# Optimization experiments

Measured on AMD Instinct MI355X. Metric: run time of the kernel, lower is better.

Reference implementation:

```python
import jax, jax.numpy as jnp
import numpy as np

TEMPERATURE = 8.0  # sqrt(d_head=64), from init_kwargs
NEG_INF = -1e9


def setup_inputs() -> dict:
    key = jax.random.key(0)
    k1, k2, k3, k4 = jax.random.split(key, 4)
    B, H, N, D = 2, 16, 2048, 64
    q = jax.random.normal(k1, (B, H, N, D), dtype=jnp.float32)
    k = jax.random.normal(k2, (B, H, N, D), dtype=jnp.float32)
    v = jax.random.normal(k3, (B, H, N, D), dtype=jnp.float32)
    mask = jax.random.randint(k4, (B, 1, N), 0, 2, dtype=jnp.int32)
    return {"q": q, "k": k, "v": v, "mask": mask}


def reference(q, k, v, mask):
    # scores: [B,H,N,N]
    attn = jnp.einsum("bhqd,bhkd->bhqk", q / TEMPERATURE, k)
    # symmetric padding mask: masked if row OR col token is masked
    m = mask.astype(attn.dtype)            # [B,1,N]
    row = m[:, :, :, None]                 # [B,1,N,1]
    col = m[:, :, None, :]                 # [B,1,1,N]
    sym = 1.0 - (1.0 - row) * (1.0 - col)  # [B,1,N,N], broadcasts over H
    attn = jnp.where(sym == 1.0, NEG_INF, attn)
    attn = jax.nn.softmax(attn, axis=-1)
    output = jnp.einsum("bhqk,bhkd->bhqd", attn, v)
    return output, attn
```

## Files before the change

kernel.cpp:

```cpp
#include <hip/hip_runtime.h>

typedef _Float16 half8 __attribute__((ext_vector_type(8)));
typedef _Float16 half4v __attribute__((ext_vector_type(4)));
typedef _Float16 half2v __attribute__((ext_vector_type(2)));
typedef float f32x4 __attribute__((ext_vector_type(4)));
typedef float f32x16 __attribute__((ext_vector_type(16)));
typedef unsigned int u32;
typedef u32 u32x2 __attribute__((ext_vector_type(2)));
typedef u32 u32x4 __attribute__((ext_vector_type(4)));
typedef int i32x4 __attribute__((ext_vector_type(4)));

#if __has_builtin(__builtin_amdgcn_exp2f)
#define EXP2F(x) __builtin_amdgcn_exp2f(x)
#else
#define EXP2F(x) exp2f(x)
#endif

#define QSCALE (1.44269504088896340736f * 0.125f)
#define NEGBIG (-16384.0f)


__device__ __forceinline__ void gload_lds16(const void* g, void* l) {
    __builtin_amdgcn_global_load_lds(
        (const __attribute__((address_space(1))) u32*)g,
        (__attribute__((address_space(3))) u32*)l, 16, 0, 0);
}

__device__ __forceinline__ void stage_tile16k(const _Float16* g, _Float16* l,
                                              int wid, int lane) {
#pragma unroll
    for (int i = 0; i < 4; ++i) {
        const int base = (wid * 4 + i) * 1024;
        gload_lds16((const char*)g + base + lane * 16, (char*)l + base);
    }
}

__device__ __forceinline__ u32 pkh(float a, float b) {
    half2v h; h[0] = (_Float16)a; h[1] = (_Float16)b;
    return __builtin_bit_cast(u32, h);
}

__device__ __forceinline__ void swap32(u32 &a, u32 &b) {
    asm volatile("v_permlane32_swap_b32 %0, %1" : "+v"(a), "+v"(b));
}


__global__ __launch_bounds__(256, 2)
void prep_kv(const float* __restrict__ kg_, const float* __restrict__ vg_,
             _Float16* __restrict__ kws_, _Float16* __restrict__ vws_)
{
    __shared__ float tile[128 * 68];
    const int tid = threadIdx.x;
    const int bh  = blockIdx.x & 31;
    const int kc  = blockIdx.x >> 5;
    const float* kg = kg_ + ((size_t)bh * 2048 + kc * 128) * 64;
    const float* vg = vg_ + ((size_t)bh * 2048 + kc * 128) * 64;
    _Float16* kt = kws_ + ((size_t)bh * 16 + kc) * 8192;
    _Float16* vt = vws_ + ((size_t)bh * 16 + kc) * 8192;

#pragma unroll
    for (int i = 0; i < 8; ++i) {
        int f = tid + 256 * i;
        int r = f >> 4, c4 = f & 15;
        f32x4 x = *reinterpret_cast<const f32x4*>(kg + r * 64 + c4 * 4);
        *reinterpret_cast<f32x4*>(&tile[r * 68 + c4 * 4]) = x;
    }
    __syncthreads();
#pragma unroll
    for (int i = 0; i < 4; ++i) {
        int s16 = tid + 256 * i;
        int R5 = s16 >> 5;
        int r  = R5 * 4 + ((s16 >> 3) & 3);
        int c  = ((s16 & 7) << 4) ^ ((R5 & 7) << 4);
        int d0 = c >> 1;
        f32x4 x0 = *reinterpret_cast<const f32x4*>(&tile[r * 68 + d0]);
        f32x4 x1 = *reinterpret_cast<const f32x4*>(&tile[r * 68 + d0 + 4]);
        half8 h;
#pragma unroll
        for (int j = 0; j < 4; ++j) { h[j] = (_Float16)x0[j]; h[4 + j] = (_Float16)x1[j]; }
        __builtin_nontemporal_store(h, reinterpret_cast<half8*>(kt + s16 * 8));
    }
    __syncthreads();
#pragma unroll
    for (int i = 0; i < 8; ++i) {
        int f = tid + 256 * i;
        int r = f >> 4, c4 = f & 15;
        f32x4 x = *reinterpret_cast<const f32x4*>(vg + r * 64 + c4 * 4);
        *reinterpret_cast<f32x4*>(&tile[r * 68 + c4 * 4]) = x;
    }
    __syncthreads();
#pragma unroll
    for (int i = 0; i < 4; ++i) {
        int s16 = tid + 256 * i;
        int R5 = s16 >> 5;
        int d  = R5 * 2 + ((s16 >> 4) & 1);
        int c  = ((s16 & 15) << 4) ^ ((R5 & 15) << 4);
        int k0 = c >> 1;
        half8 h;
#pragma unroll
        for (int j = 0; j < 8; ++j) h[j] = (_Float16)tile[(k0 + j) * 68 + d];
        __builtin_nontemporal_store(h, reinterpret_cast<half8*>(vt + s16 * 8));
    }
}

__global__ __launch_bounds__(256, 2)
void attn_sums(const float* __restrict__ qg_, const _Float16* __restrict__ kws_,
               const int* __restrict__ mg_, float* __restrict__ rsums_)
{
    __shared__ _Float16 Kb[2][8192];
    __shared__ float biasF[2048];
    const int tid = threadIdx.x, wid = tid >> 6, lane = tid & 63;
    const int l31 = lane & 31, hi = lane >> 5;
    const int bh = blockIdx.x & 31, qt = blockIdx.x >> 5;
    const int* mg = mg_ + (bh >> 4) * 2048;
    const _Float16* ktiles = kws_ + (size_t)bh * 16 * 8192;

    const float* qrow = qg_ + ((size_t)bh * 2048 + qt * 128 + wid * 32 + l31) * 64;
    half8 qf[4];
#pragma unroll
    for (int ks = 0; ks < 4; ++ks) {
        f32x4 x0 = *reinterpret_cast<const f32x4*>(qrow + ks * 16 + hi * 8);
        f32x4 x1 = *reinterpret_cast<const f32x4*>(qrow + ks * 16 + hi * 8 + 4);
#pragma unroll
        for (int j = 0; j < 4; ++j) {
            qf[ks][j]     = (_Float16)(x0[j] * QSCALE);
            qf[ks][4 + j] = (_Float16)(x1[j] * QSCALE);
        }
    }
#pragma unroll
    for (int i = 0; i < 2; ++i) {
        int j = (tid + 256 * i) * 4;
        i32x4 m = *reinterpret_cast<const i32x4*>(mg + j);
        f32x4 bv;
        bv[0] = m[0] ? NEGBIG : 0.f; bv[1] = m[1] ? NEGBIG : 0.f;
        bv[2] = m[2] ? NEGBIG : 0.f; bv[3] = m[3] ? NEGBIG : 0.f;
        *reinterpret_cast<f32x4*>(&biasF[j]) = bv;
    }
    stage_tile16k(ktiles, Kb[0], wid, lane);
    __syncthreads();

    const int rbK = (l31 >> 2) * 512 + (l31 & 3) * 128;
    const int swK = (l31 >> 2) << 4;

    float lsum = 0.f;
    _Float16 *cur = Kb[0], *nxt = Kb[1];
    for (int kc = 0; kc < 16; ++kc) {
        if (kc < 15) stage_tile16k(ktiles + (size_t)(kc + 1) * 8192, nxt, wid, lane);
        asm volatile("" ::: "memory");
        const char* curb = (const char*)cur;
#pragma unroll
        for (int kb = 0; kb < 4; ++kb) {
            f32x16 acc;
#pragma unroll
            for (int g = 0; g < 4; ++g) {
                f32x4 bv = *reinterpret_cast<const f32x4*>(
                    &biasF[kc * 128 + kb * 32 + g * 8 + hi * 4]);
                acc[4*g+0] = bv[0]; acc[4*g+1] = bv[1];
                acc[4*g+2] = bv[2]; acc[4*g+3] = bv[3];
            }
#pragma unroll
            for (int ks = 0; ks < 4; ++ks) {
                half8 kf = *reinterpret_cast<const half8*>(
                    curb + kb * 4096 + rbK + ((ks * 32 + hi * 16) ^ swK));
                acc = __builtin_amdgcn_mfma_f32_32x32x16_f16(kf, qf[ks], acc, 0, 0, 0);
            }
#pragma unroll
            for (int r = 0; r < 16; ++r) lsum += EXP2F(acc[r]);
        }
        __syncthreads();
        _Float16* t = cur; cur = nxt; nxt = t;
    }
    lsum += __shfl_xor(lsum, 32, 64);
    if (hi == 0)
        rsums_[(size_t)bh * 2048 + qt * 128 + wid * 32 + l31] = lsum;
}

__global__ __launch_bounds__(256, 2)
void attn_main(const float* __restrict__ qg_, const _Float16* __restrict__ kws_,
               const _Float16* __restrict__ vws_, const int* __restrict__ mg_,
               const float* __restrict__ rsums_,
               float* __restrict__ outg_, float* __restrict__ attng_)
{
    __shared__ _Float16 Kb[2][8192];
    __shared__ _Float16 Vb[2][8192];
    __shared__ _Float16 biasH[2048];
    __shared__ _Float16 Pb[4][32][40];
    const int tid = threadIdx.x, wid = tid >> 6, lane = tid & 63;
    const int l31 = lane & 31, hi = lane >> 5;
    const int bh = blockIdx.x & 31, qt = blockIdx.x >> 5;
    const int* mg = mg_ + (bh >> 4) * 2048;
    const _Float16* ktiles = kws_ + (size_t)bh * 16 * 8192;
    const _Float16* vtiles = vws_ + (size_t)bh * 16 * 8192;
    const int qrow_l = qt * 128 + wid * 32 + l31;

    const float* qrow = qg_ + ((size_t)bh * 2048 + qrow_l) * 64;
    half8 qf[4];
#pragma unroll
    for (int ks = 0; ks < 4; ++ks) {
        f32x4 x0 = *reinterpret_cast<const f32x4*>(qrow + ks * 16 + hi * 8);
        f32x4 x1 = *reinterpret_cast<const f32x4*>(qrow + ks * 16 + hi * 8 + 4);
#pragma unroll
        for (int j = 0; j < 4; ++j) {
            qf[ks][j]     = (_Float16)(x0[j] * QSCALE);
            qf[ks][4 + j] = (_Float16)(x1[j] * QSCALE);
        }
    }
#pragma unroll
    for (int i = 0; i < 2; ++i) {
        int j = (tid + 256 * i) * 4;
        i32x4 m = *reinterpret_cast<const i32x4*>(mg + j);
        half4v bv;
        bv[0] = m[0] ? (_Float16)NEGBIG : (_Float16)0.f;
        bv[1] = m[1] ? (_Float16)NEGBIG : (_Float16)0.f;
        bv[2] = m[2] ? (_Float16)NEGBIG : (_Float16)0.f;
        bv[3] = m[3] ? (_Float16)NEGBIG : (_Float16)0.f;
        *reinterpret_cast<half4v*>(&biasH[j]) = bv;
    }

    const float rs = rsums_[(size_t)bh * 2048 + qrow_l];
    const int   rm = mg[qrow_l];
    const bool uni = (rm != 0) || !(rs > 0.f);
    const float rscale = uni ? 0.f : 1.f / rs;
    const float radd   = uni ? (1.0f / 2048.0f) : 0.f;

    stage_tile16k(ktiles, Kb[0], wid, lane);
    stage_tile16k(vtiles, Vb[0], wid, lane);
    __syncthreads();

    f32x16 Oacc0, Oacc1;
#pragma unroll
    for (int r = 0; r < 16; ++r) { Oacc0[r] = 0.f; Oacc1[r] = 0.f; }

    float* attnw = attng_ + ((size_t)bh * 2048 + qt * 128 + wid * 32) * 2048;
    _Float16 *curK = Kb[0], *nxtK = Kb[1], *curV = Vb[0], *nxtV = Vb[1];

    const int rbK = (l31 >> 2) * 512 + (l31 & 3) * 128;
    const int swK = (l31 >> 2) << 4;
    const int rbV = (l31 >> 1) * 512 + (l31 & 1) * 256;
    const int swV = (l31 >> 1) << 4;

    for (int kc = 0; kc < 16; ++kc) {
        if (kc < 15) {
            stage_tile16k(ktiles + (size_t)(kc + 1) * 8192, nxtK, wid, lane);
            stage_tile16k(vtiles + (size_t)(kc + 1) * 8192, nxtV, wid, lane);
        }
        asm volatile("" ::: "memory");
        const char* curKb = (const char*)curK;
        const char* curVb = (const char*)curV;
#pragma unroll
        for (int kb = 0; kb < 4; ++kb) {
            f32x16 acc;
#pragma unroll
            for (int g = 0; g < 4; ++g) {
                half4v bv = *reinterpret_cast<const half4v*>(
                    &biasH[kc * 128 + kb * 32 + g * 8 + hi * 4]);
                acc[4*g+0] = (float)bv[0]; acc[4*g+1] = (float)bv[1];
                acc[4*g+2] = (float)bv[2]; acc[4*g+3] = (float)bv[3];
            }
#pragma unroll
            for (int ks = 0; ks < 4; ++ks) {
                half8 kf = *reinterpret_cast<const half8*>(
                    curKb + kb * 4096 + rbK + ((ks * 32 + hi * 16) ^ swK));
                acc = __builtin_amdgcn_mfma_f32_32x32x16_f16(kf, qf[ks], acc, 0, 0, 0);
            }
            float p[16];
#pragma unroll
            for (int r = 0; r < 16; ++r) p[r] = EXP2F(acc[r]) * rscale + radd;

            u32 wA[4], wB[4];
#pragma unroll
            for (int t = 0; t < 4; ++t) {
                wA[t] = pkh(p[4*t],     p[4*t + 1]);
                wB[t] = pkh(p[4*t + 2], p[4*t + 3]);
            }
#pragma unroll
            for (int t = 0; t < 4; ++t) {
                u32x2 ww; ww[0] = wA[t]; ww[1] = wB[t];
                *reinterpret_cast<u32x2*>(&Pb[wid][l31][t * 8 + 4 * hi]) = ww;
            }
            asm volatile("s_waitcnt lgkmcnt(0)" ::: "memory");
            __builtin_amdgcn_sched_barrier(0);

#pragma unroll
            for (int i8 = 0; i8 < 4; ++i8) {
                int rl = i8 * 8 + (lane >> 3);
                half4v ph = *reinterpret_cast<half4v*>(&Pb[wid][rl][(lane & 7) * 4]);
                f32x4 pf;
                pf[0] = (float)ph[0]; pf[1] = (float)ph[1];
                pf[2] = (float)ph[2]; pf[3] = (float)ph[3];
                __builtin_nontemporal_store(pf, reinterpret_cast<f32x4*>(
                    attnw + (size_t)rl * 2048 + kc * 128 + kb * 32 + (lane & 7) * 4));
            }

#pragma unroll
            for (int s = 0; s < 2; ++s) {
                u32 cA = wA[2*s], dA = wB[2*s], cB = wA[2*s + 1], dB = wB[2*s + 1];
                swap32(cA, cB);
                swap32(dA, dB);
                u32x4 wv; wv[0] = cA; wv[1] = dA; wv[2] = cB; wv[3] = dB;
                half8 af = __builtin_bit_cast(half8, wv);
#pragma unroll
                for (int nd = 0; nd < 2; ++nd) {
                    half8 bf = *reinterpret_cast<const half8*>(
                        curVb + nd * 8192 + rbV +
                        ((kb * 64 + s * 32 + hi * 16) ^ swV));
                    if (nd == 0) Oacc0 = __builtin_amdgcn_mfma_f32_32x32x16_f16(af, bf, Oacc0, 0, 0, 0);
                    else         Oacc1 = __builtin_amdgcn_mfma_f32_32x32x16_f16(af, bf, Oacc1, 0, 0, 0);
                }
            }
        }
        if (kc < 15) {
            asm volatile("s_waitcnt vmcnt(16) lgkmcnt(0)" ::: "memory");
            __builtin_amdgcn_s_barrier();
            _Float16* t;
            t = curK; curK = nxtK; nxtK = t;
            t = curV; curV = nxtV; nxtV = t;
        }
    }

    float* outg = outg_ + ((size_t)bh * 2048 + qt * 128) * 64;
#pragma unroll
    for (int r = 0; r < 16; ++r) {
        int q_l = wid * 32 + (r & 3) + 8 * (r >> 2) + 4 * hi;
        __builtin_nontemporal_store(Oacc0[r], outg + (size_t)q_l * 64 + l31);
        __builtin_nontemporal_store(Oacc1[r], outg + (size_t)q_l * 64 + 32 + l31);
    }
}

__global__ __launch_bounds__(256, 2)
void attn_fused(const float* __restrict__ qg_, const float* __restrict__ kg_,
                const float* __restrict__ vg_, const int* __restrict__ mg_,
                float* __restrict__ outg_, float* __restrict__ attng_)
{
    constexpr int N = 2048, D = 64, TM = 128, BK = 128, NCH = 16;
    constexpr int QS = 72, KS = 72, VTS = 136, PS = 72;
    constexpr float INVN = 1.0f / 2048.0f;

    __shared__ _Float16 Qs[TM * QS];
    __shared__ _Float16 Ksh[BK * KS];
    __shared__ _Float16 Vts[D * VTS];
    __shared__ _Float16 Ps[TM * PS];
    __shared__ unsigned char cm[N];

    const int tid  = threadIdx.x;
    const int wid  = tid >> 6;
    const int lane = tid & 63;
    const int quad = lane >> 4;
    const int l15  = lane & 15;

    const int bh = blockIdx.x & 31;
    const int qt = blockIdx.x >> 5;
    const int b  = bh >> 4;

    const float* qg = qg_ + ((size_t)bh * N + qt * TM) * D;
    const float* kg = kg_ + (size_t)bh * N * D;
    const float* vg = vg_ + (size_t)bh * N * D;
    const int*   mg = mg_ + (size_t)b * N;
    float* attng = attng_ + ((size_t)bh * N + (size_t)qt * TM) * N;
    float* outg  = outg_  + ((size_t)bh * N + qt * TM) * D;

#pragma unroll
    for (int i = 0; i < 8; ++i) {
        int f = tid + 256 * i;
        int row = f >> 4, d = (f & 15) * 4;
        float4 x = *reinterpret_cast<const float4*>(qg + (size_t)row * D + d);
        half4v hv;
        hv[0] = (_Float16)(x.x * QSCALE);
        hv[1] = (_Float16)(x.y * QSCALE);
        hv[2] = (_Float16)(x.z * QSCALE);
        hv[3] = (_Float16)(x.w * QSCALE);
        *reinterpret_cast<half4v*>(&Qs[row * QS + d]) = hv;
        cm[f] = (unsigned char)(mg[f] ? 0 : 1);
    }

    float rowm[2][4];
#pragma unroll
    for (int mb = 0; mb < 2; ++mb)
#pragma unroll
        for (int r = 0; r < 4; ++r) {
            int row = qt * TM + wid * 32 + mb * 16 + quad * 4 + r;
            rowm[mb][r] = (float)mg[row];
        }

    __syncthreads();

    half8 qfr[2][2];
#pragma unroll
    for (int mb = 0; mb < 2; ++mb)
#pragma unroll
        for (int ks = 0; ks < 2; ++ks)
            qfr[mb][ks] = *reinterpret_cast<half8*>(
                &Qs[(wid * 32 + mb * 16 + l15) * QS + ks * 32 + quad * 8]);

    float lsum[2][4] = {{0,0,0,0},{0,0,0,0}};

    for (int kc = 0; kc < NCH; ++kc) {
        __syncthreads();
#pragma unroll
        for (int i = 0; i < 8; ++i) {
            int f = tid + 256 * i;
            int row = f >> 4, d = (f & 15) * 4;
            float4 x = *reinterpret_cast<const float4*>(kg + (size_t)(kc * BK + row) * D + d);
            half4v hv;
            hv[0] = (_Float16)x.x; hv[1] = (_Float16)x.y;
            hv[2] = (_Float16)x.z; hv[3] = (_Float16)x.w;
            *reinterpret_cast<half4v*>(&Ksh[row * KS + d]) = hv;
        }
        __syncthreads();

#pragma unroll
        for (int mb = 0; mb < 2; ++mb) {
#pragma unroll
            for (int nb = 0; nb < 8; ++nb) {
                f32x4 acc = {0.f, 0.f, 0.f, 0.f};
#pragma unroll
                for (int ks = 0; ks < 2; ++ks) {
                    half8 bfr = *reinterpret_cast<half8*>(
                        &Ksh[(nb * 16 + l15) * KS + ks * 32 + quad * 8]);
                    acc = __builtin_amdgcn_mfma_f32_16x16x32_f16(qfr[mb][ks], bfr, acc, 0, 0, 0);
                }
                float cmf = (float)cm[kc * BK + nb * 16 + l15];
#pragma unroll
                for (int r = 0; r < 4; ++r)
                    lsum[mb][r] += cmf * EXP2F(acc[r]);
            }
        }
    }

#pragma unroll
    for (int mb = 0; mb < 2; ++mb)
#pragma unroll
        for (int r = 0; r < 4; ++r) {
            float s = lsum[mb][r];
            s += __shfl_xor(s, 1, 64);
            s += __shfl_xor(s, 2, 64);
            s += __shfl_xor(s, 4, 64);
            s += __shfl_xor(s, 8, 64);
            lsum[mb][r] = s;
        }

    float rscale[2][4], radd[2][4];
#pragma unroll
    for (int mb = 0; mb < 2; ++mb)
#pragma unroll
        for (int r = 0; r < 4; ++r) {
            bool uni = (rowm[mb][r] != 0.0f) || !(lsum[mb][r] > 0.0f);
            rscale[mb][r] = uni ? 0.0f : 1.0f / lsum[mb][r];
            radd[mb][r]   = uni ? INVN : 0.0f;
        }

    f32x4 Oacc[2][4];
#pragma unroll
    for (int mb = 0; mb < 2; ++mb)
#pragma unroll
        for (int nd = 0; nd < 4; ++nd)
            Oacc[mb][nd] = (f32x4){0.f, 0.f, 0.f, 0.f};

    for (int kc = 0; kc < NCH; ++kc) {
        __syncthreads();
#pragma unroll
        for (int i = 0; i < 8; ++i) {
            int f = tid + 256 * i;
            int row = f >> 4, d = (f & 15) * 4;
            float4 x = *reinterpret_cast<const float4*>(kg + (size_t)(kc * BK + row) * D + d);
            half4v hv;
            hv[0] = (_Float16)x.x; hv[1] = (_Float16)x.y;
            hv[2] = (_Float16)x.z; hv[3] = (_Float16)x.w;
            *reinterpret_cast<half4v*>(&Ksh[row * KS + d]) = hv;
        }
#pragma unroll
        for (int rr = 0; rr < 4; ++rr) {
            int key0 = rr * 32 + wid * 8;
            half8 hh;
#pragma unroll
            for (int j = 0; j < 8; ++j)
                hh[j] = (_Float16)vg[(size_t)(kc * BK + key0 + j) * D + lane];
            *reinterpret_cast<half8*>(&Vts[lane * VTS + key0]) = hh;
        }
        __syncthreads();

        f32x4 S[2][8];
#pragma unroll
        for (int mb = 0; mb < 2; ++mb)
#pragma unroll
            for (int nb = 0; nb < 8; ++nb) {
                f32x4 acc = {0.f, 0.f, 0.f, 0.f};
#pragma unroll
                for (int ks = 0; ks < 2; ++ks) {
                    half8 bfr = *reinterpret_cast<half8*>(
                        &Ksh[(nb * 16 + l15) * KS + ks * 32 + quad * 8]);
                    acc = __builtin_amdgcn_mfma_f32_16x16x32_f16(qfr[mb][ks], bfr, acc, 0, 0, 0);
                }
                S[mb][nb] = acc;
            }

#pragma unroll
        for (int h = 0; h < 2; ++h) {
#pragma unroll
            for (int nb2 = 0; nb2 < 4; ++nb2) {
                int nb = h * 4 + nb2;
                float cmf = (float)cm[kc * BK + nb * 16 + l15];
#pragma unroll
                for (int mb = 0; mb < 2; ++mb) {
#pragma unroll
                    for (int r = 0; r < 4; ++r) {
                        float p = cmf * EXP2F(S[mb][nb][r]) * rscale[mb][r] + radd[mb][r];
                        Ps[(wid * 32 + mb * 16 + quad * 4 + r) * PS + nb2 * 16 + l15] = (_Float16)p;
                    }
                }
            }
            asm volatile("s_waitcnt lgkmcnt(0)" ::: "memory");

#pragma unroll
            for (int r8 = 0; r8 < 8; ++r8) {
                int rl = r8 * 4 + quad;
                half4v ph = *reinterpret_cast<half4v*>(
                    &Ps[(wid * 32 + rl) * PS + l15 * 4]);
                f32x4 pf;
                pf[0] = (float)ph[0]; pf[1] = (float)ph[1];
                pf[2] = (float)ph[2]; pf[3] = (float)ph[3];
                float* dst = attng + (size_t)(wid * 32 + rl) * N + kc * BK + h * 64 + l15 * 4;
                __builtin_nontemporal_store(pf, reinterpret_cast<f32x4*>(dst));
            }

#pragma unroll
            for (int ks = 0; ks < 2; ++ks) {
                half8 af[2];
#pragma unroll
                for (int mb = 0; mb < 2; ++mb)
                    af[mb] = *reinterpret_cast<half8*>(
                        &Ps[(wid * 32 + mb * 16 + l15) * PS + ks * 32 + quad * 8]);
#pragma unroll
                for (int nd = 0; nd < 4; ++nd) {
                    half8 bfr = *reinterpret_cast<half8*>(
                        &Vts[(nd * 16 + l15) * VTS + h * 64 + ks * 32 + quad * 8]);
#pragma unroll
                    for (int mb = 0; mb < 2; ++mb)
                        Oacc[mb][nd] = __builtin_amdgcn_mfma_f32_16x16x32_f16(af[mb], bfr, Oacc[mb][nd], 0, 0, 0);
                }
            }
        }
    }

#pragma unroll
    for (int mb = 0; mb < 2; ++mb)
#pragma unroll
        for (int nd = 0; nd < 4; ++nd)
#pragma unroll
            for (int r = 0; r < 4; ++r)
                __builtin_nontemporal_store(
                    Oacc[mb][nd][r],
                    outg + (size_t)(wid * 32 + mb * 16 + quad * 4 + r) * D + nd * 16 + l15);
}

extern "C" void kernel_launch(void* const* d_in, const int* in_sizes, int n_in,
                              void* d_out, int out_size, void* d_ws, size_t ws_size,
                              hipStream_t stream) {
    const float* q   = (const float*)d_in[0];
    const float* k   = (const float*)d_in[1];
    const float* v   = (const float*)d_in[2];
    const int*   msk = (const int*)d_in[3];
    float* out  = (float*)d_out;
    float* attn = out + (size_t)2 * 16 * 2048 * 64;

    const size_t kv_halves = (size_t)32 * 2048 * 64;
    const size_t need = kv_halves * 2 * sizeof(_Float16)
                      + (size_t)32 * 2048 * sizeof(float);
    if (d_ws != nullptr && ws_size >= need) {
        _Float16* kws = (_Float16*)d_ws;
        _Float16* vws = kws + kv_halves;
        float* rsums  = (float*)(vws + kv_halves);
        hipLaunchKernelGGL(prep_kv,   dim3(512), dim3(256), 0, stream, k, v, kws, vws);
        hipLaunchKernelGGL(attn_sums, dim3(512), dim3(256), 0, stream, q, kws, msk, rsums);
        hipLaunchKernelGGL(attn_main, dim3(512), dim3(256), 0, stream,
                           q, kws, vws, msk, rsums, out, attn);
    } else {
        hipLaunchKernelGGL(attn_fused, dim3(512), dim3(256), 0, stream,
                           q, k, v, msk, out, attn);
    }
}
```

Baseline: 689.1 us.

## Fuse row-sum pass into main attention kernel with reverse-order second sweep

Merges the separate row-sum kernel into the main kernel: each block first sweeps K tiles to compute softmax denominators, then sweeps K/V tiles in reverse order so the last-loaded K tile is reused. This removes one kernel launch and the rsums workspace round-trip. The PV MFMAs are also moved ahead of the probability stores, and the P scratch padding is shrunk. In exchange each block now runs two sequential phases, with K loaded twice and fewer blocks available to overlap those phases.

```diff
diff --git a/kernel.cpp b/kernel.cpp
--- a/kernel.cpp
+++ b/kernel.cpp
@@ -104,87 +104,14 @@
 }
 
 __global__ __launch_bounds__(256, 2)
-void attn_sums(const float* __restrict__ qg_, const _Float16* __restrict__ kws_,
-               const int* __restrict__ mg_, float* __restrict__ rsums_)
-{
-    __shared__ _Float16 Kb[2][8192];
-    __shared__ float biasF[2048];
-    const int tid = threadIdx.x, wid = tid >> 6, lane = tid & 63;
-    const int l31 = lane & 31, hi = lane >> 5;
-    const int bh = blockIdx.x & 31, qt = blockIdx.x >> 5;
-    const int* mg = mg_ + (bh >> 4) * 2048;
-    const _Float16* ktiles = kws_ + (size_t)bh * 16 * 8192;
-
-    const float* qrow = qg_ + ((size_t)bh * 2048 + qt * 128 + wid * 32 + l31) * 64;
-    half8 qf[4];
-#pragma unroll
-    for (int ks = 0; ks < 4; ++ks) {
-        f32x4 x0 = *reinterpret_cast<const f32x4*>(qrow + ks * 16 + hi * 8);
-        f32x4 x1 = *reinterpret_cast<const f32x4*>(qrow + ks * 16 + hi * 8 + 4);
-#pragma unroll
-        for (int j = 0; j < 4; ++j) {
-            qf[ks][j]     = (_Float16)(x0[j] * QSCALE);
-            qf[ks][4 + j] = (_Float16)(x1[j] * QSCALE);
-        }
-    }
-#pragma unroll
-    for (int i = 0; i < 2; ++i) {
-        int j = (tid + 256 * i) * 4;
-        i32x4 m = *reinterpret_cast<const i32x4*>(mg + j);
-        f32x4 bv;
-        bv[0] = m[0] ? NEGBIG : 0.f; bv[1] = m[1] ? NEGBIG : 0.f;
-        bv[2] = m[2] ? NEGBIG : 0.f; bv[3] = m[3] ? NEGBIG : 0.f;
-        *reinterpret_cast<f32x4*>(&biasF[j]) = bv;
-    }
-    stage_tile16k(ktiles, Kb[0], wid, lane);
-    __syncthreads();
-
-    const int rbK = (l31 >> 2) * 512 + (l31 & 3) * 128;
-    const int swK = (l31 >> 2) << 4;
-
-    float lsum = 0.f;
-    _Float16 *cur = Kb[0], *nxt = Kb[1];
-    for (int kc = 0; kc < 16; ++kc) {
-        if (kc < 15) stage_tile16k(ktiles + (size_t)(kc + 1) * 8192, nxt, wid, lane);
-        asm volatile("" ::: "memory");
-        const char* curb = (const char*)cur;
-#pragma unroll
-        for (int kb = 0; kb < 4; ++kb) {
-            f32x16 acc;
-#pragma unroll
-            for (int g = 0; g < 4; ++g) {
-                f32x4 bv = *reinterpret_cast<const f32x4*>(
-                    &biasF[kc * 128 + kb * 32 + g * 8 + hi * 4]);
-                acc[4*g+0] = bv[0]; acc[4*g+1] = bv[1];
-                acc[4*g+2] = bv[2]; acc[4*g+3] = bv[3];
-            }
-#pragma unroll
-            for (int ks = 0; ks < 4; ++ks) {
-                half8 kf = *reinterpret_cast<const half8*>(
-                    curb + kb * 4096 + rbK + ((ks * 32 + hi * 16) ^ swK));
-                acc = __builtin_amdgcn_mfma_f32_32x32x16_f16(kf, qf[ks], acc, 0, 0, 0);
-            }
-#pragma unroll
-            for (int r = 0; r < 16; ++r) lsum += EXP2F(acc[r]);
-        }
-        __syncthreads();
-        _Float16* t = cur; cur = nxt; nxt = t;
-    }
-    lsum += __shfl_xor(lsum, 32, 64);
-    if (hi == 0)
-        rsums_[(size_t)bh * 2048 + qt * 128 + wid * 32 + l31] = lsum;
-}
-
-__global__ __launch_bounds__(256, 2)
-void attn_main(const float* __restrict__ qg_, const _Float16* __restrict__ kws_,
-               const _Float16* __restrict__ vws_, const int* __restrict__ mg_,
-               const float* __restrict__ rsums_,
-               float* __restrict__ outg_, float* __restrict__ attng_)
+void attn_ws(const float* __restrict__ qg_, const _Float16* __restrict__ kws_,
+             const _Float16* __restrict__ vws_, const int* __restrict__ mg_,
+             float* __restrict__ outg_, float* __restrict__ attng_)
 {
     __shared__ _Float16 Kb[2][8192];
     __shared__ _Float16 Vb[2][8192];
     __shared__ _Float16 biasH[2048];
-    __shared__ _Float16 Pb[4][32][40];
+    __shared__ _Float16 Pb[4][32][36];
     const int tid = threadIdx.x, wid = tid >> 6, lane = tid & 63;
     const int l31 = lane & 31, hi = lane >> 5;
     const int bh = blockIdx.x & 31, qt = blockIdx.x >> 5;
@@ -217,36 +144,20 @@
         *reinterpret_cast<half4v*>(&biasH[j]) = bv;
     }
 
-    const float rs = rsums_[(size_t)bh * 2048 + qrow_l];
-    const int   rm = mg[qrow_l];
-    const bool uni = (rm != 0) || !(rs > 0.f);
-    const float rscale = uni ? 0.f : 1.f / rs;
-    const float radd   = uni ? (1.0f / 2048.0f) : 0.f;
-
     stage_tile16k(ktiles, Kb[0], wid, lane);
-    stage_tile16k(vtiles, Vb[0], wid, lane);
     __syncthreads();
-
-    f32x16 Oacc0, Oacc1;
-#pragma unroll
-    for (int r = 0; r < 16; ++r) { Oacc0[r] = 0.f; Oacc1[r] = 0.f; }
-
-    float* attnw = attng_ + ((size_t)bh * 2048 + qt * 128 + wid * 32) * 2048;
-    _Float16 *curK = Kb[0], *nxtK = Kb[1], *curV = Vb[0], *nxtV = Vb[1];
 
     const int rbK = (l31 >> 2) * 512 + (l31 & 3) * 128;
     const int swK = (l31 >> 2) << 4;
     const int rbV = (l31 >> 1) * 512 + (l31 & 1) * 256;
     const int swV = (l31 >> 1) << 4;
 
+    float lsum = 0.f;
     for (int kc = 0; kc < 16; ++kc) {
-        if (kc < 15) {
-            stage_tile16k(ktiles + (size_t)(kc + 1) * 8192, nxtK, wid, lane);
-            stage_tile16k(vtiles + (size_t)(kc + 1) * 8192, nxtV, wid, lane);
-        }
+        if (kc < 15)
+            stage_tile16k(ktiles + (size_t)(kc + 1) * 8192, Kb[(kc + 1) & 1], wid, lane);
         asm volatile("" ::: "memory");
-        const char* curKb = (const char*)curK;
-        const char* curVb = (const char*)curV;
+        const char* curb = (const char*)Kb[kc & 1];
 #pragma unroll
         for (int kb = 0; kb < 4; ++kb) {
             f32x16 acc;
@@ -260,6 +171,55 @@
 #pragma unroll
             for (int ks = 0; ks < 4; ++ks) {
                 half8 kf = *reinterpret_cast<const half8*>(
+                    curb + kb * 4096 + rbK + ((ks * 32 + hi * 16) ^ swK));
+                acc = __builtin_amdgcn_mfma_f32_32x32x16_f16(kf, qf[ks], acc, 0, 0, 0);
+            }
+#pragma unroll
+            for (int r = 0; r < 16; ++r) lsum += EXP2F(acc[r]);
+        }
+        if (kc < 15) {
+            asm volatile("s_waitcnt vmcnt(0) lgkmcnt(0)" ::: "memory");
+            __builtin_amdgcn_s_barrier();
+        }
+    }
+
+    stage_tile16k(vtiles + (size_t)15 * 8192, Vb[1], wid, lane);
+
+    lsum += __shfl_xor(lsum, 32, 64);
+    const int  rm  = mg[qrow_l];
+    const bool uni = (rm != 0) || !(lsum > 0.f);
+    const float rscale = uni ? 0.f : 1.f / lsum;
+    const float radd   = uni ? (1.0f / 2048.0f) : 0.f;
+
+    f32x16 Oacc0, Oacc1;
+#pragma unroll
+    for (int r = 0; r < 16; ++r) { Oacc0[r] = 0.f; Oacc1[r] = 0.f; }
+
+    asm volatile("s_waitcnt vmcnt(0) lgkmcnt(0)" ::: "memory");
+    __builtin_amdgcn_s_barrier();
+
+    float* attnw = attng_ + ((size_t)bh * 2048 + qt * 128 + wid * 32) * 2048;
+    for (int kc = 15; kc >= 0; --kc) {
+        if (kc > 0) {
+            stage_tile16k(ktiles + (size_t)(kc - 1) * 8192, Kb[(kc - 1) & 1], wid, lane);
+            stage_tile16k(vtiles + (size_t)(kc - 1) * 8192, Vb[(kc - 1) & 1], wid, lane);
+        }
+        asm volatile("" ::: "memory");
+        const char* curKb = (const char*)Kb[kc & 1];
+        const char* curVb = (const char*)Vb[kc & 1];
+#pragma unroll
+        for (int kb = 0; kb < 4; ++kb) {
+            f32x16 acc;
+#pragma unroll
+            for (int g = 0; g < 4; ++g) {
+                half4v bv = *reinterpret_cast<const half4v*>(
+                    &biasH[kc * 128 + kb * 32 + g * 8 + hi * 4]);
+                acc[4*g+0] = (float)bv[0]; acc[4*g+1] = (float)bv[1];
+                acc[4*g+2] = (float)bv[2]; acc[4*g+3] = (float)bv[3];
+            }
+#pragma unroll
+            for (int ks = 0; ks < 4; ++ks) {
+                half8 kf = *reinterpret_cast<const half8*>(
                     curKb + kb * 4096 + rbK + ((ks * 32 + hi * 16) ^ swK));
                 acc = __builtin_amdgcn_mfma_f32_32x32x16_f16(kf, qf[ks], acc, 0, 0, 0);
             }
@@ -278,9 +238,25 @@
                 u32x2 ww; ww[0] = wA[t]; ww[1] = wB[t];
                 *reinterpret_cast<u32x2*>(&Pb[wid][l31][t * 8 + 4 * hi]) = ww;
             }
+
+#pragma unroll
+            for (int s = 0; s < 2; ++s) {
+                u32 cA = wA[2*s], dA = wB[2*s], cB = wA[2*s + 1], dB = wB[2*s + 1];
+                swap32(cA, cB);
+                swap32(dA, dB);
+                u32x4 wv; wv[0] = cA; wv[1] = dA; wv[2] = cB; wv[3] = dB;
+                half8 af = __builtin_bit_cast(half8, wv);
+#pragma unroll
+                for (int nd = 0; nd < 2; ++nd) {
+                    half8 bf = *reinterpret_cast<const half8*>(
+                        curVb + nd * 8192 + rbV +
+                        ((kb * 64 + s * 32 + hi * 16) ^ swV));
+                    if (nd == 0) Oacc0 = __builtin_amdgcn_mfma_f32_32x32x16_f16(af, bf, Oacc0, 0, 0, 0);
+                    else         Oacc1 = __builtin_amdgcn_mfma_f32_32x32x16_f16(af, bf, Oacc1, 0, 0, 0);
+                }
+            }
+
             asm volatile("s_waitcnt lgkmcnt(0)" ::: "memory");
-            __builtin_amdgcn_sched_barrier(0);
-
 #pragma unroll
             for (int i8 = 0; i8 < 4; ++i8) {
                 int rl = i8 * 8 + (lane >> 3);
@@ -291,30 +267,10 @@
                 __builtin_nontemporal_store(pf, reinterpret_cast<f32x4*>(
                     attnw + (size_t)rl * 2048 + kc * 128 + kb * 32 + (lane & 7) * 4));
             }
-
-#pragma unroll
-            for (int s = 0; s < 2; ++s) {
-                u32 cA = wA[2*s], dA = wB[2*s], cB = wA[2*s + 1], dB = wB[2*s + 1];
-                swap32(cA, cB);
-                swap32(dA, dB);
-                u32x4 wv; wv[0] = cA; wv[1] = dA; wv[2] = cB; wv[3] = dB;
-                half8 af = __builtin_bit_cast(half8, wv);
-#pragma unroll
-                for (int nd = 0; nd < 2; ++nd) {
-                    half8 bf = *reinterpret_cast<const half8*>(
-                        curVb + nd * 8192 + rbV +
-                        ((kb * 64 + s * 32 + hi * 16) ^ swV));
-                    if (nd == 0) Oacc0 = __builtin_amdgcn_mfma_f32_32x32x16_f16(af, bf, Oacc0, 0, 0, 0);
-                    else         Oacc1 = __builtin_amdgcn_mfma_f32_32x32x16_f16(af, bf, Oacc1, 0, 0, 0);
-                }
-            }
-        }
-        if (kc < 15) {
+        }
+        if (kc > 0) {
             asm volatile("s_waitcnt vmcnt(16) lgkmcnt(0)" ::: "memory");
             __builtin_amdgcn_s_barrier();
-            _Float16* t;
-            t = curK; curK = nxtK; nxtK = t;
-            t = curV; curV = nxtV; nxtV = t;
         }
     }
 
@@ -564,16 +520,13 @@
     float* attn = out + (size_t)2 * 16 * 2048 * 64;
 
     const size_t kv_halves = (size_t)32 * 2048 * 64;
-    const size_t need = kv_halves * 2 * sizeof(_Float16)
-                      + (size_t)32 * 2048 * sizeof(float);
+    const size_t need = kv_halves * 2 * sizeof(_Float16);
     if (d_ws != nullptr && ws_size >= need) {
         _Float16* kws = (_Float16*)d_ws;
         _Float16* vws = kws + kv_halves;
-        float* rsums  = (float*)(vws + kv_halves);
-        hipLaunchKernelGGL(prep_kv,   dim3(512), dim3(256), 0, stream, k, v, kws, vws);
-        hipLaunchKernelGGL(attn_sums, dim3(512), dim3(256), 0, stream, q, kws, msk, rsums);
-        hipLaunchKernelGGL(attn_main, dim3(512), dim3(256), 0, stream,
-                           q, kws, vws, msk, rsums, out, attn);
+        hipLaunchKernelGGL(prep_kv, dim3(512), dim3(256), 0, stream, k, v, kws, vws);
+        hipLaunchKernelGGL(attn_ws, dim3(512), dim3(256), 0, stream,
+                           q, kws, vws, msk, out, attn);
     } else {
         hipLaunchKernelGGL(attn_fused, dim3(512), dim3(256), 0, stream,
                            q, k, v, msk, out, attn);
```

After: 656.1 us. 1.05x faster.

## Split key range across two blocks with atomic accumulation of row sums and output

Applied to the files above, without the earlier changes.

Both the sum and main attention kernels now split the 16 key chunks into two halves handled by separate blocks, doubling the grid to 1024. Row sums and output are accumulated with float atomics into buffers zeroed by memsets. The main kernel also stops staging V in LDS and reads V fragments straight from global memory. It writes the probability matrix in 64-column batches and raises occupancy hints. The aim is more parallelism and higher occupancy, at the cost of extra memsets, atomic traffic and uncached V loads.

```diff
diff --git a/kernel.cpp b/kernel.cpp
--- a/kernel.cpp
+++ b/kernel.cpp
@@ -103,97 +103,21 @@
     }
 }
 
-__global__ __launch_bounds__(256, 2)
-void attn_sums(const float* __restrict__ qg_, const _Float16* __restrict__ kws_,
-               const int* __restrict__ mg_, float* __restrict__ rsums_)
+__global__ __launch_bounds__(256, 4)
+void attn_sums2(const float* __restrict__ qg_, const _Float16* __restrict__ kws_,
+                const int* __restrict__ mg_, float* __restrict__ rsums_)
 {
     __shared__ _Float16 Kb[2][8192];
-    __shared__ float biasF[2048];
+    __shared__ _Float16 biasH[2048];
     const int tid = threadIdx.x, wid = tid >> 6, lane = tid & 63;
     const int l31 = lane & 31, hi = lane >> 5;
-    const int bh = blockIdx.x & 31, qt = blockIdx.x >> 5;
+    const int bh = blockIdx.x & 31;
+    const int kh = (blockIdx.x >> 5) & 1;
+    const int qt = blockIdx.x >> 6;
     const int* mg = mg_ + (bh >> 4) * 2048;
     const _Float16* ktiles = kws_ + (size_t)bh * 16 * 8192;
 
     const float* qrow = qg_ + ((size_t)bh * 2048 + qt * 128 + wid * 32 + l31) * 64;
-    half8 qf[4];
-#pragma unroll
-    for (int ks = 0; ks < 4; ++ks) {
-        f32x4 x0 = *reinterpret_cast<const f32x4*>(qrow + ks * 16 + hi * 8);
-        f32x4 x1 = *reinterpret_cast<const f32x4*>(qrow + ks * 16 + hi * 8 + 4);
-#pragma unroll
-        for (int j = 0; j < 4; ++j) {
-            qf[ks][j]     = (_Float16)(x0[j] * QSCALE);
-            qf[ks][4 + j] = (_Float16)(x1[j] * QSCALE);
-        }
-    }
-#pragma unroll
-    for (int i = 0; i < 2; ++i) {
-        int j = (tid + 256 * i) * 4;
-        i32x4 m = *reinterpret_cast<const i32x4*>(mg + j);
-        f32x4 bv;
-        bv[0] = m[0] ? NEGBIG : 0.f; bv[1] = m[1] ? NEGBIG : 0.f;
-        bv[2] = m[2] ? NEGBIG : 0.f; bv[3] = m[3] ? NEGBIG : 0.f;
-        *reinterpret_cast<f32x4*>(&biasF[j]) = bv;
-    }
-    stage_tile16k(ktiles, Kb[0], wid, lane);
-    __syncthreads();
-
-    const int rbK = (l31 >> 2) * 512 + (l31 & 3) * 128;
-    const int swK = (l31 >> 2) << 4;
-
-    float lsum = 0.f;
-    _Float16 *cur = Kb[0], *nxt = Kb[1];
-    for (int kc = 0; kc < 16; ++kc) {
-        if (kc < 15) stage_tile16k(ktiles + (size_t)(kc + 1) * 8192, nxt, wid, lane);
-        asm volatile("" ::: "memory");
-        const char* curb = (const char*)cur;
-#pragma unroll
-        for (int kb = 0; kb < 4; ++kb) {
-            f32x16 acc;
-#pragma unroll
-            for (int g = 0; g < 4; ++g) {
-                f32x4 bv = *reinterpret_cast<const f32x4*>(
-                    &biasF[kc * 128 + kb * 32 + g * 8 + hi * 4]);
-                acc[4*g+0] = bv[0]; acc[4*g+1] = bv[1];
-                acc[4*g+2] = bv[2]; acc[4*g+3] = bv[3];
-            }
-#pragma unroll
-            for (int ks = 0; ks < 4; ++ks) {
-                half8 kf = *reinterpret_cast<const half8*>(
-                    curb + kb * 4096 + rbK + ((ks * 32 + hi * 16) ^ swK));
-                acc = __builtin_amdgcn_mfma_f32_32x32x16_f16(kf, qf[ks], acc, 0, 0, 0);
-            }
-#pragma unroll
-            for (int r = 0; r < 16; ++r) lsum += EXP2F(acc[r]);
-        }
-        __syncthreads();
-        _Float16* t = cur; cur = nxt; nxt = t;
-    }
-    lsum += __shfl_xor(lsum, 32, 64);
-    if (hi == 0)
-        rsums_[(size_t)bh * 2048 + qt * 128 + wid * 32 + l31] = lsum;
-}
-
-__global__ __launch_bounds__(256, 2)
-void attn_main(const float* __restrict__ qg_, const _Float16* __restrict__ kws_,
-               const _Float16* __restrict__ vws_, const int* __restrict__ mg_,
-               const float* __restrict__ rsums_,
-               float* __restrict__ outg_, float* __restrict__ attng_)
-{
-    __shared__ _Float16 Kb[2][8192];
-    __shared__ _Float16 Vb[2][8192];
-    __shared__ _Float16 biasH[2048];
-    __shared__ _Float16 Pb[4][32][40];
-    const int tid = threadIdx.x, wid = tid >> 6, lane = tid & 63;
-    const int l31 = lane & 31, hi = lane >> 5;
-    const int bh = blockIdx.x & 31, qt = blockIdx.x >> 5;
-    const int* mg = mg_ + (bh >> 4) * 2048;
-    const _Float16* ktiles = kws_ + (size_t)bh * 16 * 8192;
-    const _Float16* vtiles = vws_ + (size_t)bh * 16 * 8192;
-    const int qrow_l = qt * 128 + wid * 32 + l31;
-
-    const float* qrow = qg_ + ((size_t)bh * 2048 + qrow_l) * 64;
     half8 qf[4];
 #pragma unroll
     for (int ks = 0; ks < 4; ++ks) {
@@ -216,6 +140,90 @@
         bv[3] = m[3] ? (_Float16)NEGBIG : (_Float16)0.f;
         *reinterpret_cast<half4v*>(&biasH[j]) = bv;
     }
+    stage_tile16k(ktiles + (size_t)(kh * 8) * 8192, Kb[0], wid, lane);
+    __syncthreads();
+
+    const int rbK = (l31 >> 2) * 512 + (l31 & 3) * 128;
+    const int swK = (l31 >> 2) << 4;
+
+    float lsum = 0.f;
+    for (int ic = 0; ic < 8; ++ic) {
+        const int kc = kh * 8 + ic;
+        if (ic < 7)
+            stage_tile16k(ktiles + (size_t)(kc + 1) * 8192, Kb[(ic + 1) & 1], wid, lane);
+        asm volatile("" ::: "memory");
+        const char* curb = (const char*)Kb[ic & 1];
+#pragma unroll
+        for (int kb = 0; kb < 4; ++kb) {
+            f32x16 acc;
+#pragma unroll
+            for (int g = 0; g < 4; ++g) {
+                half4v bv = *reinterpret_cast<const half4v*>(
+                    &biasH[kc * 128 + kb * 32 + g * 8 + hi * 4]);
+                acc[4*g+0] = (float)bv[0]; acc[4*g+1] = (float)bv[1];
+                acc[4*g+2] = (float)bv[2]; acc[4*g+3] = (float)bv[3];
+            }
+#pragma unroll
+            for (int ks = 0; ks < 4; ++ks) {
+                half8 kf = *reinterpret_cast<const half8*>(
+                    curb + kb * 4096 + rbK + ((ks * 32 + hi * 16) ^ swK));
+                acc = __builtin_amdgcn_mfma_f32_32x32x16_f16(kf, qf[ks], acc, 0, 0, 0);
+            }
+#pragma unroll
+            for (int r = 0; r < 16; ++r) lsum += EXP2F(acc[r]);
+        }
+        if (ic < 7) {
+            asm volatile("s_waitcnt vmcnt(0) lgkmcnt(0)" ::: "memory");
+            __builtin_amdgcn_s_barrier();
+        }
+    }
+    lsum += __shfl_xor(lsum, 32, 64);
+    if (hi == 0)
+        unsafeAtomicAdd(&rsums_[(size_t)bh * 2048 + qt * 128 + wid * 32 + l31], lsum);
+}
+
+__global__ __launch_bounds__(256, 3)
+void attn_main2(const float* __restrict__ qg_, const _Float16* __restrict__ kws_,
+                const _Float16* __restrict__ vws_, const int* __restrict__ mg_,
+                const float* __restrict__ rsums_,
+                float* __restrict__ outg_, float* __restrict__ attng_)
+{
+    __shared__ _Float16 Kb[2][8192];
+    __shared__ _Float16 biasH[2048];
+    __shared__ _Float16 Pb[4][32][68];
+    const int tid = threadIdx.x, wid = tid >> 6, lane = tid & 63;
+    const int l31 = lane & 31, hi = lane >> 5;
+    const int bh = blockIdx.x & 31;
+    const int kh = (blockIdx.x >> 5) & 1;
+    const int qt = blockIdx.x >> 6;
+    const int* mg = mg_ + (bh >> 4) * 2048;
+    const _Float16* ktiles = kws_ + (size_t)bh * 16 * 8192;
+    const _Float16* vtiles = vws_ + (size_t)bh * 16 * 8192;
+    const int qrow_l = qt * 128 + wid * 32 + l31;
+
+    const float* qrow = qg_ + ((size_t)bh * 2048 + qrow_l) * 64;
+    half8 qf[4];
+#pragma unroll
+    for (int ks = 0; ks < 4; ++ks) {
+        f32x4 x0 = *reinterpret_cast<const f32x4*>(qrow + ks * 16 + hi * 8);
+        f32x4 x1 = *reinterpret_cast<const f32x4*>(qrow + ks * 16 + hi * 8 + 4);
+#pragma unroll
+        for (int j = 0; j < 4; ++j) {
+            qf[ks][j]     = (_Float16)(x0[j] * QSCALE);
+            qf[ks][4 + j] = (_Float16)(x1[j] * QSCALE);
+        }
+    }
+#pragma unroll
+    for (int i = 0; i < 2; ++i) {
+        int j = (tid + 256 * i) * 4;
+        i32x4 m = *reinterpret_cast<const i32x4*>(mg + j);
+        half4v bv;
+        bv[0] = m[0] ? (_Float16)NEGBIG : (_Float16)0.f;
+        bv[1] = m[1] ? (_Float16)NEGBIG : (_Float16)0.f;
+        bv[2] = m[2] ? (_Float16)NEGBIG : (_Float16)0.f;
+        bv[3] = m[3] ? (_Float16)NEGBIG : (_Float16)0.f;
+        *reinterpret_cast<half4v*>(&biasH[j]) = bv;
+    }
 
     const float rs = rsums_[(size_t)bh * 2048 + qrow_l];
     const int   rm = mg[qrow_l];
@@ -223,8 +231,7 @@
     const float rscale = uni ? 0.f : 1.f / rs;
     const float radd   = uni ? (1.0f / 2048.0f) : 0.f;
 
-    stage_tile16k(ktiles, Kb[0], wid, lane);
-    stage_tile16k(vtiles, Vb[0], wid, lane);
+    stage_tile16k(ktiles + (size_t)(kh * 8) * 8192, Kb[0], wid, lane);
     __syncthreads();
 
     f32x16 Oacc0, Oacc1;
@@ -232,23 +239,30 @@
     for (int r = 0; r < 16; ++r) { Oacc0[r] = 0.f; Oacc1[r] = 0.f; }
 
     float* attnw = attng_ + ((size_t)bh * 2048 + qt * 128 + wid * 32) * 2048;
-    _Float16 *curK = Kb[0], *nxtK = Kb[1], *curV = Vb[0], *nxtV = Vb[1];
 
     const int rbK = (l31 >> 2) * 512 + (l31 & 3) * 128;
     const int swK = (l31 >> 2) << 4;
     const int rbV = (l31 >> 1) * 512 + (l31 & 1) * 256;
     const int swV = (l31 >> 1) << 4;
 
-    for (int kc = 0; kc < 16; ++kc) {
-        if (kc < 15) {
-            stage_tile16k(ktiles + (size_t)(kc + 1) * 8192, nxtK, wid, lane);
-            stage_tile16k(vtiles + (size_t)(kc + 1) * 8192, nxtV, wid, lane);
-        }
+    for (int ic = 0; ic < 8; ++ic) {
+        const int kc = kh * 8 + ic;
+        if (ic < 7)
+            stage_tile16k(ktiles + (size_t)(kc + 1) * 8192, Kb[(ic + 1) & 1], wid, lane);
         asm volatile("" ::: "memory");
-        const char* curKb = (const char*)curK;
-        const char* curVb = (const char*)curV;
+        const char* curKb = (const char*)Kb[ic & 1];
+        const char* vchunk = (const char*)vtiles + (size_t)kc * 16384;
 #pragma unroll
         for (int kb = 0; kb < 4; ++kb) {
+            half8 vf[4];
+#pragma unroll
+            for (int s = 0; s < 2; ++s)
+#pragma unroll
+                for (int nd = 0; nd < 2; ++nd)
+                    vf[s * 2 + nd] = *reinterpret_cast<const half8*>(
+                        vchunk + nd * 8192 + rbV +
+                        ((kb * 64 + s * 32 + hi * 16) ^ swV));
+
             f32x16 acc;
 #pragma unroll
             for (int g = 0; g < 4; ++g) {
@@ -276,20 +290,7 @@
 #pragma unroll
             for (int t = 0; t < 4; ++t) {
                 u32x2 ww; ww[0] = wA[t]; ww[1] = wB[t];
-                *reinterpret_cast<u32x2*>(&Pb[wid][l31][t * 8 + 4 * hi]) = ww;
-            }
-            asm volatile("s_waitcnt lgkmcnt(0)" ::: "memory");
-            __builtin_amdgcn_sched_barrier(0);
-
-#pragma unroll
-            for (int i8 = 0; i8 < 4; ++i8) {
-                int rl = i8 * 8 + (lane >> 3);
-                half4v ph = *reinterpret_cast<half4v*>(&Pb[wid][rl][(lane & 7) * 4]);
-                f32x4 pf;
-                pf[0] = (float)ph[0]; pf[1] = (float)ph[1];
-                pf[2] = (float)ph[2]; pf[3] = (float)ph[3];
-                __builtin_nontemporal_store(pf, reinterpret_cast<f32x4*>(
-                    attnw + (size_t)rl * 2048 + kc * 128 + kb * 32 + (lane & 7) * 4));
+                *reinterpret_cast<u32x2*>(&Pb[wid][l31][(kb & 1) * 32 + t * 8 + 4 * hi]) = ww;
             }
 
 #pragma unroll
@@ -299,22 +300,32 @@
                 swap32(dA, dB);
                 u32x4 wv; wv[0] = cA; wv[1] = dA; wv[2] = cB; wv[3] = dB;
                 half8 af = __builtin_bit_cast(half8, wv);
-#pragma unroll
-                for (int nd = 0; nd < 2; ++nd) {
-                    half8 bf = *reinterpret_cast<const half8*>(
-                        curVb + nd * 8192 + rbV +
-                        ((kb * 64 + s * 32 + hi * 16) ^ swV));
-                    if (nd == 0) Oacc0 = __builtin_amdgcn_mfma_f32_32x32x16_f16(af, bf, Oacc0, 0, 0, 0);
-                    else         Oacc1 = __builtin_amdgcn_mfma_f32_32x32x16_f16(af, bf, Oacc1, 0, 0, 0);
+                if (s == 0) {
+                    Oacc0 = __builtin_amdgcn_mfma_f32_32x32x16_f16(af, vf[0], Oacc0, 0, 0, 0);
+                    Oacc1 = __builtin_amdgcn_mfma_f32_32x32x16_f16(af, vf[1], Oacc1, 0, 0, 0);
+                } else {
+                    Oacc0 = __builtin_amdgcn_mfma_f32_32x32x16_f16(af, vf[2], Oacc0, 0, 0, 0);
+                    Oacc1 = __builtin_amdgcn_mfma_f32_32x32x16_f16(af, vf[3], Oacc1, 0, 0, 0);
                 }
             }
-        }
-        if (kc < 15) {
+
+            if (kb & 1) {
+                asm volatile("s_waitcnt lgkmcnt(0)" ::: "memory");
+#pragma unroll
+                for (int i8 = 0; i8 < 8; ++i8) {
+                    int rl = i8 * 4 + (lane >> 4);
+                    half4v ph = *reinterpret_cast<half4v*>(&Pb[wid][rl][(lane & 15) * 4]);
+                    f32x4 pf;
+                    pf[0] = (float)ph[0]; pf[1] = (float)ph[1];
+                    pf[2] = (float)ph[2]; pf[3] = (float)ph[3];
+                    __builtin_nontemporal_store(pf, reinterpret_cast<f32x4*>(
+                        attnw + (size_t)rl * 2048 + kc * 128 + (kb >> 1) * 64 + (lane & 15) * 4));
+                }
+            }
+        }
+        if (ic < 7) {
             asm volatile("s_waitcnt vmcnt(16) lgkmcnt(0)" ::: "memory");
             __builtin_amdgcn_s_barrier();
-            _Float16* t;
-            t = curK; curK = nxtK; nxtK = t;
-            t = curV; curV = nxtV; nxtV = t;
         }
     }
 
@@ -322,8 +333,8 @@
 #pragma unroll
     for (int r = 0; r < 16; ++r) {
         int q_l = wid * 32 + (r & 3) + 8 * (r >> 2) + 4 * hi;
-        __builtin_nontemporal_store(Oacc0[r], outg + (size_t)q_l * 64 + l31);
-        __builtin_nontemporal_store(Oacc1[r], outg + (size_t)q_l * 64 + 32 + l31);
+        unsafeAtomicAdd(outg + (size_t)q_l * 64 + l31, Oacc0[r]);
+        unsafeAtomicAdd(outg + (size_t)q_l * 64 + 32 + l31, Oacc1[r]);
     }
 }
 
@@ -564,15 +575,17 @@
     float* attn = out + (size_t)2 * 16 * 2048 * 64;
 
     const size_t kv_halves = (size_t)32 * 2048 * 64;
-    const size_t need = kv_halves * 2 * sizeof(_Float16)
-                      + (size_t)32 * 2048 * sizeof(float);
+    const size_t rsum_bytes = (size_t)32 * 2048 * sizeof(float);
+    const size_t need = kv_halves * 2 * sizeof(_Float16) + rsum_bytes;
     if (d_ws != nullptr && ws_size >= need) {
         _Float16* kws = (_Float16*)d_ws;
         _Float16* vws = kws + kv_halves;
         float* rsums  = (float*)(vws + kv_halves);
-        hipLaunchKernelGGL(prep_kv,   dim3(512), dim3(256), 0, stream, k, v, kws, vws);
-        hipLaunchKernelGGL(attn_sums, dim3(512), dim3(256), 0, stream, q, kws, msk, rsums);
-        hipLaunchKernelGGL(attn_main, dim3(512), dim3(256), 0, stream,
+        hipMemsetAsync(rsums, 0, rsum_bytes, stream);
+        hipMemsetAsync(out, 0, (size_t)2 * 16 * 2048 * 64 * sizeof(float), stream);
+        hipLaunchKernelGGL(prep_kv,    dim3(512),  dim3(256), 0, stream, k, v, kws, vws);
+        hipLaunchKernelGGL(attn_sums2, dim3(1024), dim3(256), 0, stream, q, kws, msk, rsums);
+        hipLaunchKernelGGL(attn_main2, dim3(1024), dim3(256), 0, stream,
                            q, kws, vws, msk, rsums, out, attn);
     } else {
         hipLaunchKernelGGL(attn_fused, dim3(512), dim3(256), 0, stream,
```

Result: faster. 653.7 us (-5.1%).
